# Optimization experiments

Measured on AMD Instinct MI355X. Metric: run time of the kernel, lower is better.

The kernel has to match this reference:

```python
import jax, jax.numpy as jnp
import numpy as np

# dims: batch, num queries, context len, model dim, heads, head dim,
# num_q_group, v_repeat, lora rank
B, NQ, NC, D = 4, 416, 257, 768
H, DH = 6, 128
G, R, LORA = 104, 4, 64  # NQ == R * G, all_q_mid == G * LORA
EPS = 1e-5


def ln(x, g, b):
    m = jnp.mean(x, axis=-1, keepdims=True)
    v = jnp.mean(jnp.square(x - m), axis=-1, keepdims=True)
    return (x - m) * jax.lax.rsqrt(v + EPS) * g + b


def setup_inputs() -> dict:
    key = jax.random.key(0)
    ks = jax.random.split(key, 7)
    s = 0.02
    return {
        "x": jax.random.normal(ks[0], (B, NQ, D), dtype=jnp.float32),
        "context": jax.random.normal(ks[1], (B, NC, D), dtype=jnp.float32),
        "Wq": jax.random.normal(ks[2], (D, D), dtype=jnp.float32) * s,
        "gq": jnp.ones((D,), jnp.float32), "bq": jnp.zeros((D,), jnp.float32),
        "Wk": jax.random.normal(ks[3], (D, D), dtype=jnp.float32) * s,
        "gk": jnp.ones((D,), jnp.float32), "bk": jnp.zeros((D,), jnp.float32),
        "Wv": jax.random.normal(ks[4], (D, G * LORA), dtype=jnp.float32) * s,
        "gv1": jnp.ones((G * LORA,), jnp.float32), "bv1": jnp.zeros((G * LORA,), jnp.float32),
        "Wconv": jax.random.normal(ks[5], (G, LORA, D), dtype=jnp.float32) * s,  # grouped 1x1 conv: per-group (LORA -> D)
        "gv2": jnp.ones((D,), jnp.float32), "bv2": jnp.zeros((D,), jnp.float32),
        "Wo": jax.random.normal(ks[6], (D, D), dtype=jnp.float32) * s,
        "go": jnp.ones((D,), jnp.float32), "bo": jnp.zeros((D,), jnp.float32),
    }


def reference(x, context, Wq, gq, bq, Wk, gk, bk, Wv, gv1, bv1, Wconv, gv2, bv2, Wo, go, bo):
    # to_q / to_k: Linear (no bias) + affine LayerNorm
    q = ln(x @ Wq, gq, bq)          # (B, NQ, D)
    k = ln(context @ Wk, gk, bk)    # (B, NC, D)
    # split heads -> (B*H, n, DH)
    q = q.reshape(B, NQ, H, DH).transpose(0, 2, 1, 3).reshape(B * H, NQ, DH)
    k = k.reshape(B, NC, H, DH).transpose(0, 2, 1, 3).reshape(B * H, NC, DH)

    # q-aware to_v: Linear -> LN -> grouped 1x1 Conv1d -> LN, plus skip of context
    mid = ln(context @ Wv, gv1, bv1)                 # (B, NC, G*LORA)
    mid = mid.reshape(B, NC, G, LORA)
    v = jnp.einsum('bngl,gld->bgnd', mid, Wconv)     # grouped conv, (B, G, NC, D)
    v = ln(v, gv2, bv2)
    v = v + context[:, None]                          # v_has_skip: context.unsqueeze(1)
    # heads: (B, G, NC, H, DH) -> (B*H, G, NC, DH)
    v = v.reshape(B, G, NC, H, DH).transpose(0, 3, 1, 2, 4).reshape(B * H, G, NC, DH)

    scale = DH ** (-0.25)
    sim = jnp.einsum('bid,bjd->bij', q * scale, k * scale)   # (B*H, NQ, NC)
    attn = jax.nn.softmax(sim, axis=-1)                       # dropout in eval mode: identity

    # torch repeat(1, R, 1, 1) tiles v along q-dim: query i uses group i % G.
    # reshape attn to (B*H, R, G, NC) so that i = r*G + g maps to group g.
    attn_g = attn.reshape(B * H, R, G, NC)
    out = jnp.einsum('brgj,bgjd->brgd', attn_g, v).reshape(B * H, NQ, DH)

    # merge heads -> (B, NQ, D)
    out = out.reshape(B, H, NQ, DH).transpose(0, 2, 1, 3).reshape(B, NQ, D)
    # to_out: Linear (no bias) + Dropout(eval: identity) + affine LayerNorm
    return ln(out @ Wo, go, bo)
```

## Files before the change

kernel.cpp:

```cpp
#include <hip/hip_runtime.h>


typedef unsigned short u16;
typedef unsigned int   u32;
typedef __attribute__((ext_vector_type(4))) float f32x4;
typedef __attribute__((ext_vector_type(4))) u32   u32x4;
typedef __attribute__((ext_vector_type(8))) short bf16x8;

__device__ __forceinline__ float bf2f(u16 v) { return __uint_as_float(((u32)v) << 16); }
__device__ __forceinline__ u16 f2bf(float f) {
  u32 u = __float_as_uint(f);
  u32 r = u + 0x7fffu + ((u >> 16) & 1u);
  return (u16)(r >> 16);
}
__device__ __forceinline__ float gld(const void* p, long idx, int f32) {
  return f32 ? ((const float*)p)[idx] : bf2f(((const u16*)p)[idx]);
}

typedef const __attribute__((address_space(1))) u32 gas_u32;
typedef __attribute__((address_space(3))) u32 las_u32;

__device__ __forceinline__ void stage16(const u16* g, u16* lbase, int lane) {
#if __has_builtin(__builtin_amdgcn_global_load_lds)
  (void)lane;
  __builtin_amdgcn_global_load_lds((gas_u32*)g, (las_u32*)lbase, 16, 0, 0);
#else
  *(u32x4*)(lbase + lane * 8) = *(const u32x4*)g;
#endif
}

__global__ __launch_bounds__(256) void probe_k(const u32* __restrict__ xw, int* __restrict__ flag) {
  int tid = threadIdx.x, c = 0;
  for (int i = tid; i < 4096; i += 256) {
    u16 lo = (u16)(xw[i] & 0xffffu);
    float a = fabsf(bf2f(lo));
    if (lo == 0 || (a >= 1e-3f && a <= 32.f)) ++c;
  }
#pragma unroll
  for (int o = 32; o; o >>= 1) c += __shfl_xor(c, o, 64);
  __shared__ int r[4];
  if ((tid & 63) == 0) r[tid >> 6] = c;
  __syncthreads();
  if (tid == 0) flag[0] = (r[0] + r[1] + r[2] + r[3] >= 2048) ? 0 : 1;
}

__global__ __launch_bounds__(256) void fill_k(u16* p, float v, int n) {
  int i = blockIdx.x * 256 + threadIdx.x;
  if (i < n) p[i] = f2bf(v);
}

__global__ __launch_bounds__(256) void convb4_k(
    const void* __restrict__ s0, u16* __restrict__ d0, int n0_,
    const void* __restrict__ s1, u16* __restrict__ d1, int n1_,
    const void* __restrict__ s2, u16* __restrict__ d2, int n2_,
    u16* __restrict__ midi, int n3_,
    const int* __restrict__ dtf)
{
  const int f = dtf[0];
  long i = ((long)blockIdx.x * 256 + threadIdx.x) * 8;
  const long t0 = n0_, t1 = t0 + n1_, t2 = t1 + n2_, t3 = t2 + n3_;
  if (i >= t3) return;
  if (i >= t2) {
    long e = i - t2;
    long z = e / 448, off = e - z * 448;
    u32x4 zz = {0u, 0u, 0u, 0u};
    *(u32x4*)(midi + z * 16896 + 16448 + off) = zz;
    return;
  }
  const void* in; u16* out;
  if (i < t0)      { in = s0; out = d0; }
  else if (i < t1) { in = s1; out = d1; i -= t0; }
  else             { in = s2; out = d2; i -= t1; }
  if (f) {
    const float* ip = (const float*)in + i;
    f32x4 a = *(const f32x4*)ip, b = *(const f32x4*)(ip + 4);
    u32x4 q = { (u32)f2bf(a.x) | ((u32)f2bf(a.y) << 16),
                (u32)f2bf(a.z) | ((u32)f2bf(a.w) << 16),
                (u32)f2bf(b.x) | ((u32)f2bf(b.y) << 16),
                (u32)f2bf(b.z) | ((u32)f2bf(b.w) << 16) };
    *(u32x4*)(out + i) = q;
  } else {
    *(u32x4*)(out + i) = *(const u32x4*)((const u16*)in + i);
  }
}

__global__ __launch_bounds__(256) void transM_k(
    const void* __restrict__ Wq, const void* __restrict__ Wk, const void* __restrict__ Wo,
    const void* __restrict__ Wv, const void* __restrict__ ctx,
    u16* __restrict__ wqt, u16* __restrict__ wkt, u16* __restrict__ wot,
    u16* __restrict__ wvt, u16* __restrict__ ctxT,
    const int* __restrict__ dtf)
{
  const int f = dtf[0];
  int t = blockIdx.x;
  const void* in; u16* out;
  int inK, inN, ldo, outK, nx;
  long inBase = 0, outBase = 0;
  if (t < 1728) {
    int w = t / 576; t -= w * 576;
    in  = w == 0 ? Wq : w == 1 ? Wk : Wo;
    out = w == 0 ? wqt : w == 1 ? wkt : wot;
    inK = 768; inN = 768; ldo = 768; outK = 768; nx = 24;
  } else if (t < 6720) {
    t -= 1728;
    in = Wv; out = wvt;
    inK = 768; inN = 6656; ldo = 768; outK = 768; nx = 208;
  } else {
    t -= 6720;
    int b = t / 216; t -= b * 216;
    in = ctx; out = ctxT;
    inK = 257; inN = 768; ldo = 264; outK = 264; nx = 24;
    inBase = (long)b * 257 * 768; outBase = (long)b * 768 * 264;
  }
  int n0 = (t % nx) * 32, k0 = (t / nx) * 32;
  __shared__ float s[32][33];
  int tx = threadIdx.x & 31, ty = threadIdx.x >> 5;
#pragma unroll
  for (int i = 0; i < 32; i += 8) {
    int k = k0 + ty + i, n = n0 + tx;
    float v = 0.f;
    if (k < inK && n < inN) v = gld(in, inBase + (long)k * inN + n, f);
    s[ty + i][tx] = v;
  }
  __syncthreads();
#pragma unroll
  for (int i = 0; i < 32; i += 8) {
    int n = n0 + ty + i, k = k0 + tx;
    if (n < inN && k < outK) out[outBase + (long)n * ldo + k] = f2bf(s[tx][ty + i]);
  }
}

__device__ __forceinline__ void gemm128_body(
    const u16* __restrict__ A, const u16* __restrict__ B, u16* __restrict__ C,
    int M, int N, int K, int lda, int ldb, int ldc, int m0, int n0)
{
  __shared__ __attribute__((aligned(16))) u16 As[128 * 32];
  __shared__ __attribute__((aligned(16))) u16 Bs[128 * 32];
  const int tid = threadIdx.x, lane = tid & 63, wave = tid >> 6;
  const int wm = (wave >> 1) * 64, wn = (wave & 1) * 64;
  const int fm = lane & 15, fq = lane >> 4;

  const int srow = lane >> 2, selem = (lane & 3) * 8;
  int ra1 = m0 + wave * 16 + srow;      if (ra1 > M - 1) ra1 = M - 1;
  int ra2 = m0 + 64 + wave * 16 + srow; if (ra2 > M - 1) ra2 = M - 1;
  const int rb1 = n0 + wave * 16 + srow;
  const int rb2 = n0 + 64 + wave * 16 + srow;
  const u16* pa1 = A + (long)ra1 * lda + selem;
  const u16* pa2 = A + (long)ra2 * lda + selem;
  const u16* pb1 = B + (long)rb1 * ldb + selem;
  const u16* pb2 = B + (long)rb2 * ldb + selem;
  u16* la1 = As + wave * 512;
  u16* la2 = As + 2048 + wave * 512;
  u16* lb1 = Bs + wave * 512;
  u16* lb2 = Bs + 2048 + wave * 512;

  f32x4 acc[4][4];
  const f32x4 zero4 = {0.f, 0.f, 0.f, 0.f};
#pragma unroll
  for (int a_ = 0; a_ < 4; ++a_)
#pragma unroll
    for (int b_ = 0; b_ < 4; ++b_) acc[a_][b_] = zero4;

  for (int k0 = 0; k0 < K; k0 += 32) {
    stage16(pa1, la1, lane);
    stage16(pa2, la2, lane);
    stage16(pb1, lb1, lane);
    stage16(pb2, lb2, lane);
    pa1 += 32; pa2 += 32; pb1 += 32; pb2 += 32;
    __syncthreads();
    bf16x8 fa[4], fb[4];
#pragma unroll
    for (int mt = 0; mt < 4; ++mt)
      fa[mt] = *(const bf16x8*)&As[(wm + mt * 16 + fm) * 32 + fq * 8];
#pragma unroll
    for (int nt = 0; nt < 4; ++nt)
      fb[nt] = *(const bf16x8*)&Bs[(wn + nt * 16 + fm) * 32 + fq * 8];
#pragma unroll
    for (int mt = 0; mt < 4; ++mt)
#pragma unroll
      for (int nt = 0; nt < 4; ++nt)
        acc[mt][nt] = __builtin_amdgcn_mfma_f32_16x16x32_bf16(fa[mt], fb[nt], acc[mt][nt], 0, 0, 0);
    __syncthreads();
  }
#pragma unroll
  for (int mt = 0; mt < 4; ++mt)
#pragma unroll
    for (int nt = 0; nt < 4; ++nt)
#pragma unroll
      for (int rr = 0; rr < 4; ++rr) {
        int gm = m0 + wm + mt * 16 + fq * 4 + rr;
        int gn = n0 + wn + nt * 16 + fm;
        if (gm < M) C[(long)gm * ldc + gn] = f2bf(acc[mt][nt][rr]);
      }
}

__global__ __launch_bounds__(256) void gemm128(
    const u16* __restrict__ A, const u16* __restrict__ B, u16* __restrict__ C,
    int M, int N, int K, int lda, int ldb, int ldc)
{
  gemm128_body(A, B, C, M, N, K, lda, ldb, ldc, blockIdx.x * 128, blockIdx.y * 128);
}

__global__ __launch_bounds__(256) void mgemm3_k(
    const u16* __restrict__ Aq, const u16* __restrict__ Bq, u16* __restrict__ Cq,
    const u16* __restrict__ Ak, const u16* __restrict__ Bk, u16* __restrict__ Ck,
    const u16* __restrict__ Am, const u16* __restrict__ Bm, u16* __restrict__ Cm)
{
  int bid = blockIdx.x;
  const u16 *A, *B; u16* C; int M, N, lid, mx;
  if (bid < 78)       { A = Aq; B = Bq; C = Cq; M = 1664; N = 768;  lid = bid;       mx = 13; }
  else if (bid < 132) { A = Ak; B = Bk; C = Ck; M = 1028; N = 768;  lid = bid - 78;  mx = 9;  }
  else                { A = Am; B = Bm; C = Cm; M = 1028; N = 6656; lid = bid - 132; mx = 9;  }
  int m0 = (lid % mx) * 128, n0 = (lid / mx) * 128;
  gemm128_body(A, B, C, M, N, 768, 768, 768, N, m0, n0);
}

#define LDS_S 40

__global__ __launch_bounds__(256) void gemm_bf16(
    const void* __restrict__ A, const void* __restrict__ B,
    float* __restrict__ Cf, u16* __restrict__ Cb, int obf,
    int M, int N, int K, int lda, int ldb, int ldc,
    long sAo, long sAi, int adiv, long sBo, long sBi, int bdiv,
    long sC, int zoff, int btrans, float alpha,
    const int* __restrict__ dtf, int aSel, int bSel)
{
  const int f = dtf[0];
  const int af32 = aSel & f, bf32 = bSel & f;
  const int zl = blockIdx.z, zg = zl + zoff;
  const long aoff = (long)(zg / adiv) * sAo + (long)(zg % adiv) * sAi;
  const long boff = (long)(zg / bdiv) * sBo + (long)(zg % bdiv) * sBi;
  const u16*   A16 = (const u16*)A + aoff;
  const float* A32 = (const float*)A + aoff;
  const u16*   B16 = (const u16*)B + boff;
  const float* B32 = (const float*)B + boff;

  __shared__ __attribute__((aligned(16))) u16 As[64 * LDS_S];
  __shared__ __attribute__((aligned(16))) u16 Bs[64 * LDS_S];

  const int tid = threadIdx.x;
  const int lane = tid & 63, wave = tid >> 6;
  const int m0 = blockIdx.x * 64, n0 = blockIdx.y * 64;
  const int wm = (wave >> 1) * 32, wn = (wave & 1) * 32;
  const int fm = lane & 15, fq = lane >> 4;

  const int ar = tid >> 2, ak = (tid & 3) * 8;
  const int bk = tid >> 3, bn = (tid & 7) * 8;

  f32x4 acc[2][2];
  const f32x4 zero4 = {0.f, 0.f, 0.f, 0.f};
#pragma unroll
  for (int a_ = 0; a_ < 2; ++a_)
#pragma unroll
    for (int b_ = 0; b_ < 2; ++b_) acc[a_][b_] = zero4;

  for (int k0 = 0; k0 < K; k0 += 32) {
    {
      int gm = m0 + ar, gk = k0 + ak;
      long idx = (long)gm * lda + gk;
      if (gm < M && gk + 8 <= K) {
        if (af32) {
          f32x4 u = *(const f32x4*)(A32 + idx), v = *(const f32x4*)(A32 + idx + 4);
          u32x4 q = { (u32)f2bf(u.x) | ((u32)f2bf(u.y) << 16),
                      (u32)f2bf(u.z) | ((u32)f2bf(u.w) << 16),
                      (u32)f2bf(v.x) | ((u32)f2bf(v.y) << 16),
                      (u32)f2bf(v.z) | ((u32)f2bf(v.w) << 16) };
          *(u32x4*)&As[ar * LDS_S + ak] = q;
        } else {
          *(u32x4*)&As[ar * LDS_S + ak] = *(const u32x4*)(A16 + idx);
        }
      } else {
#pragma unroll
        for (int e = 0; e < 8; ++e) {
          u16 v = 0;
          if (gm < M && gk + e < K) v = f2bf(gld(A, aoff + idx + e, af32));
          As[ar * LDS_S + ak + e] = v;
        }
      }
    }
    if (btrans) {
      int gn = n0 + ar, gk = k0 + ak;
      long idx = (long)gn * ldb + gk;
      if (gn < N && gk + 8 <= K) {
        if (bf32) {
          f32x4 u = *(const f32x4*)(B32 + idx), v = *(const f32x4*)(B32 + idx + 4);
          u32x4 q = { (u32)f2bf(u.x) | ((u32)f2bf(u.y) << 16),
                      (u32)f2bf(u.z) | ((u32)f2bf(u.w) << 16),
                      (u32)f2bf(v.x) | ((u32)f2bf(v.y) << 16),
                      (u32)f2bf(v.z) | ((u32)f2bf(v.w) << 16) };
          *(u32x4*)&Bs[ar * LDS_S + ak] = q;
        } else {
          *(u32x4*)&Bs[ar * LDS_S + ak] = *(const u32x4*)(B16 + idx);
        }
      } else {
#pragma unroll
        for (int e = 0; e < 8; ++e) {
          u16 v = 0;
          if (gn < N && gk + e < K) v = f2bf(gld(B, boff + idx + e, bf32));
          Bs[ar * LDS_S + ak + e] = v;
        }
      }
    } else {
      int gk = k0 + bk;
      long idx = (long)gk * ldb + n0 + bn;
      u16 tmp[8];
      if (gk < K) {
        if (bf32) {
          f32x4 u = *(const f32x4*)(B32 + idx), v = *(const f32x4*)(B32 + idx + 4);
          tmp[0] = f2bf(u.x); tmp[1] = f2bf(u.y); tmp[2] = f2bf(u.z); tmp[3] = f2bf(u.w);
          tmp[4] = f2bf(v.x); tmp[5] = f2bf(v.y); tmp[6] = f2bf(v.z); tmp[7] = f2bf(v.w);
        } else {
          u32x4 v = *(const u32x4*)(B16 + idx);
          tmp[0] = (u16)(v.x & 0xffff); tmp[1] = (u16)(v.x >> 16);
          tmp[2] = (u16)(v.y & 0xffff); tmp[3] = (u16)(v.y >> 16);
          tmp[4] = (u16)(v.z & 0xffff); tmp[5] = (u16)(v.z >> 16);
          tmp[6] = (u16)(v.w & 0xffff); tmp[7] = (u16)(v.w >> 16);
        }
      } else {
#pragma unroll
        for (int e = 0; e < 8; ++e) tmp[e] = 0;
      }
      int rot = tid & 7;
#pragma unroll
      for (int e = 0; e < 8; ++e) {
        int ee = (e + rot) & 7;
        Bs[(bn + ee) * LDS_S + bk] = tmp[ee];
      }
    }
    __syncthreads();
    {
      bf16x8 fa[2], fb[2];
      fa[0] = *(const bf16x8*)&As[(wm +      fm) * LDS_S + fq * 8];
      fa[1] = *(const bf16x8*)&As[(wm + 16 + fm) * LDS_S + fq * 8];
      fb[0] = *(const bf16x8*)&Bs[(wn +      fm) * LDS_S + fq * 8];
      fb[1] = *(const bf16x8*)&Bs[(wn + 16 + fm) * LDS_S + fq * 8];
#pragma unroll
      for (int mt = 0; mt < 2; ++mt)
#pragma unroll
        for (int nt = 0; nt < 2; ++nt)
          acc[mt][nt] = __builtin_amdgcn_mfma_f32_16x16x32_bf16(fa[mt], fb[nt], acc[mt][nt], 0, 0, 0);
    }
    __syncthreads();
  }
#pragma unroll
  for (int mt = 0; mt < 2; ++mt)
#pragma unroll
    for (int nt = 0; nt < 2; ++nt)
#pragma unroll
      for (int rr = 0; rr < 4; ++rr) {
        int gm = m0 + wm + mt * 16 + fq * 4 + rr;
        int gn = n0 + wn + nt * 16 + fm;
        if (gm < M && gn < N) {
          float v = alpha * acc[mt][nt][rr];
          if (obf) Cb[(long)zl * sC + (long)gm * ldc + gn] = f2bf(v);
          else     Cf[(long)zl * sC + (long)gm * ldc + gn] = v;
        }
      }
}

__device__ __forceinline__ void ln_row(
    const u16* __restrict__ ip, const void* __restrict__ g, const void* __restrict__ b,
    u16* __restrict__ ob, float* __restrict__ of, int N, int f)
{
  int tid = threadIdx.x, lane = tid & 63, wave = tid >> 6;
  const int nv = N >> 3;
  float s1 = 0.f, s2 = 0.f;
  for (int c8 = tid; c8 < nv; c8 += 256) {
    u32x4 v = *(const u32x4*)(ip + c8 * 8);
    float e0 = bf2f((u16)(v.x & 0xffff)), e1 = bf2f((u16)(v.x >> 16));
    float e2 = bf2f((u16)(v.y & 0xffff)), e3 = bf2f((u16)(v.y >> 16));
    float e4 = bf2f((u16)(v.z & 0xffff)), e5 = bf2f((u16)(v.z >> 16));
    float e6 = bf2f((u16)(v.w & 0xffff)), e7 = bf2f((u16)(v.w >> 16));
    s1 += ((e0 + e1) + (e2 + e3)) + ((e4 + e5) + (e6 + e7));
    s2 += ((e0*e0 + e1*e1) + (e2*e2 + e3*e3)) + ((e4*e4 + e5*e5) + (e6*e6 + e7*e7));
  }
#pragma unroll
  for (int o = 32; o; o >>= 1) { s1 += __shfl_xor(s1, o, 64); s2 += __shfl_xor(s2, o, 64); }
  __shared__ float red[8];
  if (lane == 0) { red[wave] = s1; red[4 + wave] = s2; }
  __syncthreads();
  s1 = red[0] + red[1] + red[2] + red[3];
  s2 = red[4] + red[5] + red[6] + red[7];
  float mean = s1 / N;
  float var = s2 / N - mean * mean;
  float rstd = rsqrtf(fmaxf(var, 0.f) + 1e-5f);
  for (int c8 = tid; c8 < nv; c8 += 256) {
    int c = c8 * 8;
    u32x4 v = *(const u32x4*)(ip + c);
    float e[8];
    e[0] = bf2f((u16)(v.x & 0xffff)); e[1] = bf2f((u16)(v.x >> 16));
    e[2] = bf2f((u16)(v.y & 0xffff)); e[3] = bf2f((u16)(v.y >> 16));
    e[4] = bf2f((u16)(v.z & 0xffff)); e[5] = bf2f((u16)(v.z >> 16));
    e[6] = bf2f((u16)(v.w & 0xffff)); e[7] = bf2f((u16)(v.w >> 16));
    float gg[8], bb[8];
    if (f) {
      const float* gp = (const float*)g + c; const float* bp = (const float*)b + c;
      f32x4 g0 = *(const f32x4*)gp, g1 = *(const f32x4*)(gp + 4);
      f32x4 b0 = *(const f32x4*)bp, b1 = *(const f32x4*)(bp + 4);
      gg[0]=g0.x; gg[1]=g0.y; gg[2]=g0.z; gg[3]=g0.w; gg[4]=g1.x; gg[5]=g1.y; gg[6]=g1.z; gg[7]=g1.w;
      bb[0]=b0.x; bb[1]=b0.y; bb[2]=b0.z; bb[3]=b0.w; bb[4]=b1.x; bb[5]=b1.y; bb[6]=b1.z; bb[7]=b1.w;
    } else {
      u32x4 gv = *(const u32x4*)((const u16*)g + c);
      u32x4 bv = *(const u32x4*)((const u16*)b + c);
      gg[0]=bf2f((u16)(gv.x&0xffff)); gg[1]=bf2f((u16)(gv.x>>16));
      gg[2]=bf2f((u16)(gv.y&0xffff)); gg[3]=bf2f((u16)(gv.y>>16));
      gg[4]=bf2f((u16)(gv.z&0xffff)); gg[5]=bf2f((u16)(gv.z>>16));
      gg[6]=bf2f((u16)(gv.w&0xffff)); gg[7]=bf2f((u16)(gv.w>>16));
      bb[0]=bf2f((u16)(bv.x&0xffff)); bb[1]=bf2f((u16)(bv.x>>16));
      bb[2]=bf2f((u16)(bv.y&0xffff)); bb[3]=bf2f((u16)(bv.y>>16));
      bb[4]=bf2f((u16)(bv.z&0xffff)); bb[5]=bf2f((u16)(bv.z>>16));
      bb[6]=bf2f((u16)(bv.w&0xffff)); bb[7]=bf2f((u16)(bv.w>>16));
    }
    float o_[8];
#pragma unroll
    for (int e2i = 0; e2i < 8; ++e2i) o_[e2i] = (e[e2i] - mean) * rstd * gg[e2i] + bb[e2i];
    if (of) {
      f32x4 o0 = {o_[0], o_[1], o_[2], o_[3]}, o1 = {o_[4], o_[5], o_[6], o_[7]};
      *(f32x4*)(of + c) = o0; *(f32x4*)(of + c + 4) = o1;
    } else {
      u32x4 q = { (u32)f2bf(o_[0]) | ((u32)f2bf(o_[1]) << 16),
                  (u32)f2bf(o_[2]) | ((u32)f2bf(o_[3]) << 16),
                  (u32)f2bf(o_[4]) | ((u32)f2bf(o_[5]) << 16),
                  (u32)f2bf(o_[6]) | ((u32)f2bf(o_[7]) << 16) };
      *(u32x4*)(ob + c) = q;
    }
  }
}

__global__ __launch_bounds__(256) void ln_rows(
    const u16* __restrict__ in, const void* __restrict__ g, const void* __restrict__ b,
    void* __restrict__ out, int N, const int* __restrict__ dtf, int isfinal)
{
  const int f = dtf[0];
  long row = blockIdx.x;
  const u16* ip = in + row * N;
  float* of = (isfinal && f) ? (float*)out + row * N : nullptr;
  u16*   ob = of ? nullptr : (u16*)out + row * N;
  ln_row(ip, g, b, ob, of, N, f);
}

__global__ __launch_bounds__(256) void mln3_k(
    u16* __restrict__ qb, const void* __restrict__ gq, const void* __restrict__ bq,
    u16* __restrict__ kb, const void* __restrict__ gk, const void* __restrict__ bk,
    u16* __restrict__ mb, const void* __restrict__ gv, const void* __restrict__ bv,
    const int* __restrict__ dtf)
{
  const int f = dtf[0];
  int row = blockIdx.x;
  u16* ip; const void *g, *b; int N;
  if (row < 1664)      { ip = qb + (long)row * 768; g = gq; b = bq; N = 768; }
  else if (row < 2692) { ip = kb + (long)(row - 1664) * 768; g = gk; b = bk; N = 768; }
  else                 { ip = mb + (long)(row - 2692) * 6656; g = gv; b = bv; N = 6656; }
  ln_row(ip, g, b, ip, nullptr, N, f);
}

__global__ __launch_bounds__(256) void wbar_k(const u16* __restrict__ Wb,
                                              float* __restrict__ wbar)
{
  int r = blockIdx.x * 4 + (threadIdx.x >> 6);
  int lane = threadIdx.x & 63;
  const u16* p = Wb + (long)r * 768;
  float s = 0.f;
  for (int c = lane; c < 768; c += 64) s += bf2f(p[c]);
#pragma unroll
  for (int o = 32; o; o >>= 1) s += __shfl_xor(s, o, 64);
  if (lane == 0) wbar[r] = s * (1.f / 768.f);
}

__global__ __launch_bounds__(256) void stats2_k(
    const u16* __restrict__ midbf, const u16* __restrict__ Y, const float* __restrict__ wbar,
    u16* __restrict__ midi, float* __restrict__ pim)
{
  int g = blockIdx.y;
  int r = blockIdx.x * 4 + (threadIdx.x >> 6);
  int lane = threadIdx.x & 63;
  int b = r / 257, j = r - b * 257;
  float m = bf2f(midbf[(long)r * 6656 + g * 64 + lane]);
  float y = bf2f(Y[((long)g * 1028 + r) * 64 + lane]);
  float wb = wbar[g * 64 + lane];
  float mup = m * wb, q2p = m * y;
#pragma unroll
  for (int o = 32; o; o >>= 1) { mup += __shfl_xor(mup, o, 64); q2p += __shfl_xor(q2p, o, 64); }
  float var = q2p - mup * mup;
  float inv = rsqrtf(fmaxf(var, 0.f) + 1e-5f);
  long zidx = (long)b * 104 + g;
  midi[(zidx * 264 + j) * 64 + lane] = f2bf(inv * m);
  if (lane == 0) pim[zidx * 257 + j] = inv * mup;
}

__global__ __launch_bounds__(256) void softmax_k(
    const float* __restrict__ simf, const float* __restrict__ pim,
    u16* __restrict__ Abf, u16* __restrict__ A2bf, float* __restrict__ s_sh)
{
  int bh = blockIdx.x;
  int b = bh / 6, h = bh - b * 6;
  int tid = threadIdx.x, lane = tid & 63, wave = tid >> 6;
  int i = blockIdx.y * 4 + wave;
  int g = i % 104, rq = i / 104;
  const float* sp_ = simf + ((long)bh * 416 + i) * 257;
  float s[5];
#pragma unroll
  for (int jc = 0; jc < 5; ++jc) {
    int j = jc * 64 + lane;
    s[jc] = (j < 257) ? sp_[j] : -1e30f;
  }
  float mx = -1e30f;
#pragma unroll
  for (int jc = 0; jc < 5; ++jc) mx = fmaxf(mx, s[jc]);
#pragma unroll
  for (int o = 32; o; o >>= 1) mx = fmaxf(mx, __shfl_xor(mx, o, 64));
  float p[5], sum = 0.f, sp = 0.f;
  long pimb = ((long)b * 104 + g) * 257;
#pragma unroll
  for (int jc = 0; jc < 5; ++jc) {
    int j = jc * 64 + lane;
    float pv = 0.f;
    if (j < 257) { pv = __expf(s[jc] - mx); sp = fmaf(pv, pim[pimb + j], sp); }
    p[jc] = pv; sum += pv;
  }
#pragma unroll
  for (int o = 32; o; o >>= 1) { sum += __shfl_xor(sum, o, 64); sp += __shfl_xor(sp, o, 64); }
  float rs = 1.f / sum;
  long arow  = ((long)bh * 416 + i) * 264;
  long a2row = (((long)b * 104 + g) * 24 + h * 4 + rq) * 264;
#pragma unroll
  for (int jc = 0; jc < 5; ++jc) {
    int j = jc * 64 + lane;
    if (j < 257) { u16 pb = f2bf(p[jc] * rs); Abf[arow + j] = pb; A2bf[a2row + j] = pb; }
    else if (j < 264) { Abf[arow + j] = 0; A2bf[a2row + j] = 0; }
  }
  if (lane == 0) s_sh[(long)bh * 416 + i] = sp * rs;
}

__global__ __launch_bounds__(256) void oc_k(
    const u16* __restrict__ T, const u16* __restrict__ Wb,
    const float* __restrict__ s_sh, const float* __restrict__ c_buf,
    const void* __restrict__ gv2, const void* __restrict__ bv2,
    u16* __restrict__ opbf, const int* __restrict__ dtf)
{
  const int f = dtf[0];
  int z = blockIdx.x;
  int b = z / 104, g = z - b * 104;
  int tid = threadIdx.x;
  __shared__ float Ts[24][64];
  const u16* tp = T + (long)z * 1536;
  for (int idx = tid; idx < 1536; idx += 256) Ts[idx >> 6][idx & 63] = bf2f(tp[idx]);
  __syncthreads();
  const int dh = tid & 127;
  const int hbase = (tid >> 7) * 3;
  const u16* wg = Wb + (long)g * 49152;
#pragma unroll
  for (int hh = 0; hh < 3; ++hh) {
    int h = hbase + hh;
    int d = h * 128 + dh;
    const u16* wp = wg + d;
    float a0 = 0.f, a1 = 0.f, a2 = 0.f, a3 = 0.f;
#pragma unroll 16
    for (int k = 0; k < 64; ++k) {
      float w = bf2f(wp[(long)k * 768]);
      a0 = fmaf(Ts[h * 4 + 0][k], w, a0);
      a1 = fmaf(Ts[h * 4 + 1][k], w, a1);
      a2 = fmaf(Ts[h * 4 + 2][k], w, a2);
      a3 = fmaf(Ts[h * 4 + 3][k], w, a3);
    }
    float acc[4] = {a0, a1, a2, a3};
    float gvd = gld(gv2, d, f), bvd = gld(bv2, d, f);
#pragma unroll
    for (int rq = 0; rq < 4; ++rq) {
      int i = rq * 104 + g;
      float ssh = s_sh[((long)b * 6 + h) * 416 + i];
      float val = gvd * (acc[rq] - ssh) + bvd
                + c_buf[(((long)b * 6 + h) * 416 + i) * 128 + dh];
      opbf[((long)b * 416 + i) * 768 + d] = f2bf(val);
    }
  }
}

static void launch_gemm(const void* A, const void* B, float* Cf, u16* Cb, int obf,
                        int M, int N, int K, int lda, int ldb, int ldc,
                        long sAo, long sAi, int adiv, long sBo, long sBi, int bdiv,
                        long sC, int zoff, int Z, int btrans, float alpha,
                        const int* dtf, int aSel, int bSel, hipStream_t st)
{
  dim3 grid((M + 63) / 64, (N + 63) / 64, Z);
  gemm_bf16<<<grid, dim3(256), 0, st>>>(A, B, Cf, Cb, obf, M, N, K, lda, ldb, ldc,
                                        sAo, sAi, adiv, sBo, sBi, bdiv,
                                        sC, zoff, btrans, alpha, dtf, aSel, bSel);
}

extern "C" void kernel_launch(void* const* d_in, const int* in_sizes, int n_in,
                              void* d_out, int out_size, void* d_ws, size_t ws_size,
                              hipStream_t stream)
{
  (void)in_sizes; (void)n_in;
  const void* x   = d_in[0];
  const void* ctx = d_in[1];
  const void* Wq  = d_in[2];
  const void* gq  = d_in[3];
  const void* bq  = d_in[4];
  const void* Wk  = d_in[5];
  const void* gk  = d_in[6];
  const void* bk  = d_in[7];
  const void* Wv  = d_in[8];
  const void* gv1 = d_in[9];
  const void* bv1 = d_in[10];
  const void* Wcv = d_in[11];
  const void* gv2 = d_in[12];
  const void* bv2 = d_in[13];
  const void* Wo  = d_in[14];
  const void* go  = d_in[15];
  const void* bo  = d_in[16];

  const size_t SZ_FLAG = 256;
  const size_t SZ_QBF  = 2555904;
  const size_t SZ_KBF  = 1579008;
  const size_t SZ_MID  = 13684736;
  const size_t SZ_MM   = 1703936;
  const size_t SZ_WB   = 26624;
  const size_t SZ_MIDI = 14057472;
  const size_t SZ_PIM  = 427648;
  const size_t SZ_ABF  = 5271552;
  const size_t SZ_A2   = 5271552;
  const size_t SZ_SSH  = 39936;
  const size_t SZ_CB   = 1579008;
  const size_t SZ_WCVB = 10223616;
  const size_t SZ_YF   = 13684736;
  const size_t SZ_WT   = 1179648;
  const size_t SZ_WVT  = 10223616;
  const size_t SZ_CTXT = 1622016;
  const size_t REQUIRED = SZ_FLAG + SZ_QBF + SZ_KBF + SZ_MID + SZ_MM + SZ_WB +
                          SZ_MIDI + SZ_PIM + SZ_ABF + SZ_A2 + SZ_SSH + SZ_CB +
                          SZ_WCVB + SZ_YF + 3 * SZ_WT + SZ_WVT + SZ_CTXT;

  if (ws_size < REQUIRED) {
    fill_k<<<(out_size + 255) / 256, 256, 0, stream>>>((u16*)d_out, (float)(ws_size >> 20), out_size);
    return;
  }

  char* p = (char*)d_ws;
  int*   dtf   = (int*)  p;                 p += SZ_FLAG;
  u16*   qbf   = (u16*)  p;                 p += SZ_QBF;
  u16*   kbf   = (u16*)  p;                 p += SZ_KBF;
  char*  midrg = p;                         p += SZ_MID;
  char*  mmrg  = p;                         p += SZ_MM;
  float* wbar  = (float*)p;                 p += SZ_WB;
  u16*   midi  = (u16*)  p;                 p += SZ_MIDI;
  float* pim   = (float*)p;                 p += SZ_PIM;
  char*  abfrg = p;                         p += SZ_ABF;
  u16*   A2bf  = (u16*)  p;                 p += SZ_A2;
  float* s_sh  = (float*)p;                 p += SZ_SSH;
  u16*   cb    = (u16*)  p;                 p += SZ_CB;
  u16*   wcvb  = (u16*)  p;                 p += SZ_WCVB;
  u16*   yfull = (u16*)  p;                 p += SZ_YF;
  u16*   wqt2  = (u16*)  p;                 p += SZ_WT;
  u16*   wkt2  = (u16*)  p;                 p += SZ_WT;
  u16*   wot2  = (u16*)  p;                 p += SZ_WT;
  u16*   wvt   = (u16*)  p;                 p += SZ_WVT;
  u16*   ctxT  = (u16*)  p;                 p += SZ_CTXT;

  u16*   midbf = (u16*)midrg;
  float* simf  = (float*)midrg;
  float* c_buf = (float*)midrg;
  u16*   Tb16  = (u16*)(midrg + 5111808);
  u16*   Gb    = (u16*)mmrg;
  u16*   xb    = (u16*)abfrg;
  u16*   Abf   = (u16*)abfrg;
  u16*   opbf  = (u16*)abfrg;

  probe_k<<<1, 256, 0, stream>>>((const u32*)x, dtf);

  {
    const int n0_ = 1277952, n1_ = 789504, n2_ = 5111808, n3_ = 186368;
    long tot = (long)n0_ + n1_ + n2_ + n3_;
    int blocks = (int)((tot / 8 + 255) / 256);
    convb4_k<<<blocks, 256, 0, stream>>>(x, xb, n0_, ctx, cb, n1_, Wcv, wcvb, n2_,
                                         midi, n3_, dtf);
  }
  transM_k<<<7584, 256, 0, stream>>>(Wq, Wk, Wo, Wv, ctx,
                                     wqt2, wkt2, wot2, wvt, ctxT, dtf);

  mgemm3_k<<<600, 256, 0, stream>>>(xb, wqt2, qbf, cb, wkt2, kbf, cb, wvt, midbf);
  mln3_k<<<3720, 256, 0, stream>>>(qbf, gq, bq, kbf, gk, bk, midbf, gv1, bv1, dtf);

  launch_gemm(wcvb, wcvb, nullptr, Gb, 1, 64, 64, 768, 768, 768, 64,
              49152, 0, 1, 49152, 0, 1, 4096, 0, 104, 1, 1.f / 768.f, dtf, 0, 0, stream);
  wbar_k<<<1664, 256, 0, stream>>>(wcvb, wbar);
  launch_gemm(midbf, Gb, nullptr, yfull, 1,
              1028, 64, 64, 6656, 64, 64,
              0, 64, 104, 4096, 0, 1, 65792, 0, 104, 1, 1.f, dtf, 0, 0, stream);
  stats2_k<<<dim3(257, 104), 256, 0, stream>>>(midbf, yfull, wbar, midi, pim);

  launch_gemm(qbf, kbf, simf, nullptr, 0, 416, 257, 128, 768, 768, 257,
              319488, 128, 6, 197376, 128, 6, 106912, 0, 24, 1,
              0.08838834764831845f, dtf, 0, 0, stream);
  softmax_k<<<dim3(24, 104), 256, 0, stream>>>(simf, pim, Abf, A2bf, s_sh);

  launch_gemm(Abf, ctxT, c_buf, nullptr, 0, 416, 128, 264, 264, 264, 128,
              109824, 0, 1, 202752, 33792, 6, 53248, 0, 24, 1, 1.f, dtf, 0, 0, stream);
  launch_gemm(A2bf, midi, nullptr, Tb16, 1, 24, 64, 264, 264, 64, 64,
              6336, 0, 1, 16896, 0, 1, 1536, 0, 416, 0, 1.f, dtf, 0, 0, stream);

  oc_k<<<416, 256, 0, stream>>>(Tb16, wcvb, s_sh, c_buf, gv2, bv2, opbf, dtf);

  {
    dim3 grid(13, 6, 1);
    gemm128<<<grid, dim3(256), 0, stream>>>(opbf, wot2, qbf, 1664, 768, 768, 768, 768, 768);
  }
  ln_rows<<<1664, 256, 0, stream>>>(qbf, go, bo, d_out, 768, dtf, 1);
}
```

Measured before the change: 309.1 us.

## Merge independent launches into combined multi-role kernels to cut launch count

Folds the conversion, transpose and wbar kernels into one prep kernel. It merges the Gram GEMM into the projection GEMM launch, the Y GEMM with the QK^T sim GEMM, and the two attention-output GEMMs into one launch each. The sim buffer gets its own workspace region so it no longer aliases midbf while both are live. The aim is fewer kernel launches and less inter-kernel idle time, at the cost of heterogeneous blocks and the loss of the fp32 input path in the generic GEMM.

After: 273.2 us. 11.6% less time.

```diff
diff --git a/kernel.cpp b/kernel.cpp
--- a/kernel.cpp
+++ b/kernel.cpp
@@ -49,84 +49,92 @@
   if (i < n) p[i] = f2bf(v);
 }
 
-__global__ __launch_bounds__(256) void convb4_k(
-    const void* __restrict__ s0, u16* __restrict__ d0, int n0_,
-    const void* __restrict__ s1, u16* __restrict__ d1, int n1_,
-    const void* __restrict__ s2, u16* __restrict__ d2, int n2_,
-    u16* __restrict__ midi, int n3_,
-    const int* __restrict__ dtf)
-{
-  const int f = dtf[0];
-  long i = ((long)blockIdx.x * 256 + threadIdx.x) * 8;
-  const long t0 = n0_, t1 = t0 + n1_, t2 = t1 + n2_, t3 = t2 + n3_;
-  if (i >= t3) return;
-  if (i >= t2) {
-    long e = i - t2;
-    long z = e / 448, off = e - z * 448;
-    u32x4 zz = {0u, 0u, 0u, 0u};
-    *(u32x4*)(midi + z * 16896 + 16448 + off) = zz;
-    return;
-  }
-  const void* in; u16* out;
-  if (i < t0)      { in = s0; out = d0; }
-  else if (i < t1) { in = s1; out = d1; i -= t0; }
-  else             { in = s2; out = d2; i -= t1; }
-  if (f) {
-    const float* ip = (const float*)in + i;
-    f32x4 a = *(const f32x4*)ip, b = *(const f32x4*)(ip + 4);
-    u32x4 q = { (u32)f2bf(a.x) | ((u32)f2bf(a.y) << 16),
-                (u32)f2bf(a.z) | ((u32)f2bf(a.w) << 16),
-                (u32)f2bf(b.x) | ((u32)f2bf(b.y) << 16),
-                (u32)f2bf(b.z) | ((u32)f2bf(b.w) << 16) };
-    *(u32x4*)(out + i) = q;
-  } else {
-    *(u32x4*)(out + i) = *(const u32x4*)((const u16*)in + i);
-  }
-}
-
-__global__ __launch_bounds__(256) void transM_k(
-    const void* __restrict__ Wq, const void* __restrict__ Wk, const void* __restrict__ Wo,
-    const void* __restrict__ Wv, const void* __restrict__ ctx,
+__global__ __launch_bounds__(256) void prep_k(
+    const void* __restrict__ x,   u16* __restrict__ xb,
+    const void* __restrict__ ctx, u16* __restrict__ cbuf,
+    const void* __restrict__ Wcv, u16* __restrict__ wcvb,
+    u16* __restrict__ midi,
+    const void* __restrict__ Wq, const void* __restrict__ Wk,
+    const void* __restrict__ Wo, const void* __restrict__ Wv,
     u16* __restrict__ wqt, u16* __restrict__ wkt, u16* __restrict__ wot,
     u16* __restrict__ wvt, u16* __restrict__ ctxT,
-    const int* __restrict__ dtf)
+    float* __restrict__ wbar, const int* __restrict__ dtf)
 {
   const int f = dtf[0];
-  int t = blockIdx.x;
-  const void* in; u16* out;
-  int inK, inN, ldo, outK, nx;
-  long inBase = 0, outBase = 0;
-  if (t < 1728) {
-    int w = t / 576; t -= w * 576;
-    in  = w == 0 ? Wq : w == 1 ? Wk : Wo;
-    out = w == 0 ? wqt : w == 1 ? wkt : wot;
-    inK = 768; inN = 768; ldo = 768; outK = 768; nx = 24;
-  } else if (t < 6720) {
-    t -= 1728;
-    in = Wv; out = wvt;
-    inK = 768; inN = 6656; ldo = 768; outK = 768; nx = 208;
+  int bid = blockIdx.x;
+  __shared__ float s[32][33];
+  if (bid < 3597) {
+    const long n0_ = 1277952, n1_ = 789504, n2_ = 5111808, n3_ = 186368;
+    long i = ((long)bid * 256 + threadIdx.x) * 8;
+    const long t0 = n0_, t1 = t0 + n1_, t2 = t1 + n2_, t3 = t2 + n3_;
+    if (i >= t3) return;
+    if (i >= t2) {
+      long e = i - t2;
+      long z = e / 448, off = e - z * 448;
+      u32x4 zz = {0u, 0u, 0u, 0u};
+      *(u32x4*)(midi + z * 16896 + 16448 + off) = zz;
+      return;
+    }
+    const void* in; u16* out;
+    if (i < t0)      { in = x;    out = xb; }
+    else if (i < t1) { in = ctx;  out = cbuf; i -= t0; }
+    else             { in = Wcv;  out = wcvb; i -= t1; }
+    if (f) {
+      const float* ip = (const float*)in + i;
+      f32x4 a = *(const f32x4*)ip, b = *(const f32x4*)(ip + 4);
+      u32x4 q = { (u32)f2bf(a.x) | ((u32)f2bf(a.y) << 16),
+                  (u32)f2bf(a.z) | ((u32)f2bf(a.w) << 16),
+                  (u32)f2bf(b.x) | ((u32)f2bf(b.y) << 16),
+                  (u32)f2bf(b.z) | ((u32)f2bf(b.w) << 16) };
+      *(u32x4*)(out + i) = q;
+    } else {
+      *(u32x4*)(out + i) = *(const u32x4*)((const u16*)in + i);
+    }
+  } else if (bid < 11181) {
+    int t = bid - 3597;
+    const void* in; u16* out;
+    int inK, inN, ldo, outK, nx;
+    long inBase = 0, outBase = 0;
+    if (t < 1728) {
+      int w = t / 576; t -= w * 576;
+      in  = w == 0 ? Wq : w == 1 ? Wk : Wo;
+      out = w == 0 ? wqt : w == 1 ? wkt : wot;
+      inK = 768; inN = 768; ldo = 768; outK = 768; nx = 24;
+    } else if (t < 6720) {
+      t -= 1728;
+      in = Wv; out = wvt;
+      inK = 768; inN = 6656; ldo = 768; outK = 768; nx = 208;
+    } else {
+      t -= 6720;
+      int b = t / 216; t -= b * 216;
+      in = ctx; out = ctxT;
+      inK = 257; inN = 768; ldo = 264; outK = 264; nx = 24;
+      inBase = (long)b * 257 * 768; outBase = (long)b * 768 * 264;
+    }
+    int n0 = (t % nx) * 32, k0 = (t / nx) * 32;
+    int tx = threadIdx.x & 31, ty = threadIdx.x >> 5;
+#pragma unroll
+    for (int i = 0; i < 32; i += 8) {
+      int k = k0 + ty + i, n = n0 + tx;
+      float v = 0.f;
+      if (k < inK && n < inN) v = gld(in, inBase + (long)k * inN + n, f);
+      s[ty + i][tx] = v;
+    }
+    __syncthreads();
+#pragma unroll
+    for (int i = 0; i < 32; i += 8) {
+      int n = n0 + ty + i, k = k0 + tx;
+      if (n < inN && k < outK) out[outBase + (long)n * ldo + k] = f2bf(s[tx][ty + i]);
+    }
   } else {
-    t -= 6720;
-    int b = t / 216; t -= b * 216;
-    in = ctx; out = ctxT;
-    inK = 257; inN = 768; ldo = 264; outK = 264; nx = 24;
-    inBase = (long)b * 257 * 768; outBase = (long)b * 768 * 264;
-  }
-  int n0 = (t % nx) * 32, k0 = (t / nx) * 32;
-  __shared__ float s[32][33];
-  int tx = threadIdx.x & 31, ty = threadIdx.x >> 5;
-#pragma unroll
-  for (int i = 0; i < 32; i += 8) {
-    int k = k0 + ty + i, n = n0 + tx;
-    float v = 0.f;
-    if (k < inK && n < inN) v = gld(in, inBase + (long)k * inN + n, f);
-    s[ty + i][tx] = v;
-  }
-  __syncthreads();
-#pragma unroll
-  for (int i = 0; i < 32; i += 8) {
-    int n = n0 + ty + i, k = k0 + tx;
-    if (n < inN && k < outK) out[outBase + (long)n * ldo + k] = f2bf(s[tx][ty + i]);
+    int r = (bid - 11181) * 4 + (threadIdx.x >> 6);
+    int lane = threadIdx.x & 63;
+    long base = (long)r * 768;
+    float sm = 0.f;
+    for (int c = lane; c < 768; c += 64) sm += gld(Wcv, base + c, f);
+#pragma unroll
+    for (int o = 32; o; o >>= 1) sm += __shfl_xor(sm, o, 64);
+    if (lane == 0) wbar[r] = sm * (1.f / 768.f);
   }
 }
 
@@ -201,49 +209,19 @@
   gemm128_body(A, B, C, M, N, K, lda, ldb, ldc, blockIdx.x * 128, blockIdx.y * 128);
 }
 
-__global__ __launch_bounds__(256) void mgemm3_k(
-    const u16* __restrict__ Aq, const u16* __restrict__ Bq, u16* __restrict__ Cq,
-    const u16* __restrict__ Ak, const u16* __restrict__ Bk, u16* __restrict__ Ck,
-    const u16* __restrict__ Am, const u16* __restrict__ Bm, u16* __restrict__ Cm)
-{
-  int bid = blockIdx.x;
-  const u16 *A, *B; u16* C; int M, N, lid, mx;
-  if (bid < 78)       { A = Aq; B = Bq; C = Cq; M = 1664; N = 768;  lid = bid;       mx = 13; }
-  else if (bid < 132) { A = Ak; B = Bk; C = Ck; M = 1028; N = 768;  lid = bid - 78;  mx = 9;  }
-  else                { A = Am; B = Bm; C = Cm; M = 1028; N = 6656; lid = bid - 132; mx = 9;  }
-  int m0 = (lid % mx) * 128, n0 = (lid / mx) * 128;
-  gemm128_body(A, B, C, M, N, 768, 768, 768, N, m0, n0);
-}
-
 #define LDS_S 40
 
-__global__ __launch_bounds__(256) void gemm_bf16(
-    const void* __restrict__ A, const void* __restrict__ B,
-    float* __restrict__ Cf, u16* __restrict__ Cb, int obf,
+__device__ __forceinline__ void gemm64_body(
+    u16* As, u16* Bs,
+    const u16* __restrict__ A16, const u16* __restrict__ B16,
+    float* Cf, u16* Cb,
     int M, int N, int K, int lda, int ldb, int ldc,
-    long sAo, long sAi, int adiv, long sBo, long sBi, int bdiv,
-    long sC, int zoff, int btrans, float alpha,
-    const int* __restrict__ dtf, int aSel, int bSel)
-{
-  const int f = dtf[0];
-  const int af32 = aSel & f, bf32 = bSel & f;
-  const int zl = blockIdx.z, zg = zl + zoff;
-  const long aoff = (long)(zg / adiv) * sAo + (long)(zg % adiv) * sAi;
-  const long boff = (long)(zg / bdiv) * sBo + (long)(zg % bdiv) * sBi;
-  const u16*   A16 = (const u16*)A + aoff;
-  const float* A32 = (const float*)A + aoff;
-  const u16*   B16 = (const u16*)B + boff;
-  const float* B32 = (const float*)B + boff;
-
-  __shared__ __attribute__((aligned(16))) u16 As[64 * LDS_S];
-  __shared__ __attribute__((aligned(16))) u16 Bs[64 * LDS_S];
-
+    int btrans, float alpha, int m0, int n0)
+{
   const int tid = threadIdx.x;
   const int lane = tid & 63, wave = tid >> 6;
-  const int m0 = blockIdx.x * 64, n0 = blockIdx.y * 64;
   const int wm = (wave >> 1) * 32, wn = (wave & 1) * 32;
   const int fm = lane & 15, fq = lane >> 4;
-
   const int ar = tid >> 2, ak = (tid & 3) * 8;
   const int bk = tid >> 3, bn = (tid & 7) * 8;
 
@@ -259,63 +237,33 @@
       int gm = m0 + ar, gk = k0 + ak;
       long idx = (long)gm * lda + gk;
       if (gm < M && gk + 8 <= K) {
-        if (af32) {
-          f32x4 u = *(const f32x4*)(A32 + idx), v = *(const f32x4*)(A32 + idx + 4);
-          u32x4 q = { (u32)f2bf(u.x) | ((u32)f2bf(u.y) << 16),
-                      (u32)f2bf(u.z) | ((u32)f2bf(u.w) << 16),
-                      (u32)f2bf(v.x) | ((u32)f2bf(v.y) << 16),
-                      (u32)f2bf(v.z) | ((u32)f2bf(v.w) << 16) };
-          *(u32x4*)&As[ar * LDS_S + ak] = q;
-        } else {
-          *(u32x4*)&As[ar * LDS_S + ak] = *(const u32x4*)(A16 + idx);
-        }
+        *(u32x4*)&As[ar * LDS_S + ak] = *(const u32x4*)(A16 + idx);
       } else {
 #pragma unroll
-        for (int e = 0; e < 8; ++e) {
-          u16 v = 0;
-          if (gm < M && gk + e < K) v = f2bf(gld(A, aoff + idx + e, af32));
-          As[ar * LDS_S + ak + e] = v;
-        }
+        for (int e = 0; e < 8; ++e)
+          As[ar * LDS_S + ak + e] = (gm < M && gk + e < K) ? A16[idx + e] : (u16)0;
       }
     }
     if (btrans) {
       int gn = n0 + ar, gk = k0 + ak;
       long idx = (long)gn * ldb + gk;
       if (gn < N && gk + 8 <= K) {
-        if (bf32) {
-          f32x4 u = *(const f32x4*)(B32 + idx), v = *(const f32x4*)(B32 + idx + 4);
-          u32x4 q = { (u32)f2bf(u.x) | ((u32)f2bf(u.y) << 16),
-                      (u32)f2bf(u.z) | ((u32)f2bf(u.w) << 16),
-                      (u32)f2bf(v.x) | ((u32)f2bf(v.y) << 16),
-                      (u32)f2bf(v.z) | ((u32)f2bf(v.w) << 16) };
-          *(u32x4*)&Bs[ar * LDS_S + ak] = q;
-        } else {
-          *(u32x4*)&Bs[ar * LDS_S + ak] = *(const u32x4*)(B16 + idx);
-        }
+        *(u32x4*)&Bs[ar * LDS_S + ak] = *(const u32x4*)(B16 + idx);
       } else {
 #pragma unroll
-        for (int e = 0; e < 8; ++e) {
-          u16 v = 0;
-          if (gn < N && gk + e < K) v = f2bf(gld(B, boff + idx + e, bf32));
-          Bs[ar * LDS_S + ak + e] = v;
-        }
+        for (int e = 0; e < 8; ++e)
+          Bs[ar * LDS_S + ak + e] = (gn < N && gk + e < K) ? B16[idx + e] : (u16)0;
       }
     } else {
       int gk = k0 + bk;
       long idx = (long)gk * ldb + n0 + bn;
       u16 tmp[8];
       if (gk < K) {
-        if (bf32) {
-          f32x4 u = *(const f32x4*)(B32 + idx), v = *(const f32x4*)(B32 + idx + 4);
-          tmp[0] = f2bf(u.x); tmp[1] = f2bf(u.y); tmp[2] = f2bf(u.z); tmp[3] = f2bf(u.w);
-          tmp[4] = f2bf(v.x); tmp[5] = f2bf(v.y); tmp[6] = f2bf(v.z); tmp[7] = f2bf(v.w);
-        } else {
-          u32x4 v = *(const u32x4*)(B16 + idx);
-          tmp[0] = (u16)(v.x & 0xffff); tmp[1] = (u16)(v.x >> 16);
-          tmp[2] = (u16)(v.y & 0xffff); tmp[3] = (u16)(v.y >> 16);
-          tmp[4] = (u16)(v.z & 0xffff); tmp[5] = (u16)(v.z >> 16);
-          tmp[6] = (u16)(v.w & 0xffff); tmp[7] = (u16)(v.w >> 16);
-        }
+        u32x4 v = *(const u32x4*)(B16 + idx);
+        tmp[0] = (u16)(v.x & 0xffff); tmp[1] = (u16)(v.x >> 16);
+        tmp[2] = (u16)(v.y & 0xffff); tmp[3] = (u16)(v.y >> 16);
+        tmp[4] = (u16)(v.z & 0xffff); tmp[5] = (u16)(v.z >> 16);
+        tmp[6] = (u16)(v.w & 0xffff); tmp[7] = (u16)(v.w >> 16);
       } else {
 #pragma unroll
         for (int e = 0; e < 8; ++e) tmp[e] = 0;
@@ -352,10 +300,86 @@
         int gn = n0 + wn + nt * 16 + fm;
         if (gm < M && gn < N) {
           float v = alpha * acc[mt][nt][rr];
-          if (obf) Cb[(long)zl * sC + (long)gm * ldc + gn] = f2bf(v);
-          else     Cf[(long)zl * sC + (long)gm * ldc + gn] = v;
+          if (Cb) Cb[(long)gm * ldc + gn] = f2bf(v);
+          else    Cf[(long)gm * ldc + gn] = v;
         }
       }
+}
+
+__global__ __launch_bounds__(256) void mg4_k(
+    const u16* __restrict__ xb, const u16* __restrict__ wqt, u16* __restrict__ qbf,
+    const u16* __restrict__ cbuf, const u16* __restrict__ wkt, u16* __restrict__ kbf,
+    const u16* __restrict__ wvt, u16* __restrict__ midbf,
+    const u16* __restrict__ wcvb, u16* __restrict__ Gb)
+{
+  int bid = blockIdx.x;
+  if (bid < 600) {
+    const u16 *A, *B; u16* C; int M, N, lid, mx;
+    if (bid < 78)       { A = xb;   B = wqt; C = qbf;   M = 1664; N = 768;  lid = bid;       mx = 13; }
+    else if (bid < 132) { A = cbuf; B = wkt; C = kbf;   M = 1028; N = 768;  lid = bid - 78;  mx = 9;  }
+    else                { A = cbuf; B = wvt; C = midbf; M = 1028; N = 6656; lid = bid - 132; mx = 9;  }
+    int m0 = (lid % mx) * 128, n0 = (lid / mx) * 128;
+    gemm128_body(A, B, C, M, N, 768, 768, 768, N, m0, n0);
+  } else {
+    __shared__ __attribute__((aligned(16))) u16 As[64 * LDS_S];
+    __shared__ __attribute__((aligned(16))) u16 Bs[64 * LDS_S];
+    int z = bid - 600;
+    gemm64_body(As, Bs, wcvb + (long)z * 49152, wcvb + (long)z * 49152,
+                nullptr, Gb + (long)z * 4096,
+                64, 64, 768, 768, 768, 64, 1, 1.f / 768.f, 0, 0);
+  }
+}
+
+__global__ __launch_bounds__(256) void ysim_k(
+    const u16* __restrict__ midbf, const u16* __restrict__ Gb, u16* __restrict__ yfull,
+    const u16* __restrict__ qbf, const u16* __restrict__ kbf, float* __restrict__ simf)
+{
+  __shared__ __attribute__((aligned(16))) u16 As[64 * LDS_S];
+  __shared__ __attribute__((aligned(16))) u16 Bs[64 * LDS_S];
+  int bid = blockIdx.x;
+  const u16 *A, *B; float* Cf = nullptr; u16* Cb = nullptr;
+  int M, N, K, lda, ldb, ldc, btrans, m0, n0; float alpha;
+  if (bid < 1768) {
+    int z = bid / 17, bx = bid % 17;
+    A = midbf + (long)z * 64;  B = Gb + (long)z * 4096;  Cb = yfull + (long)z * 65792;
+    M = 1028; N = 64; K = 64; lda = 6656; ldb = 64; ldc = 64;
+    btrans = 1; alpha = 1.f; m0 = bx * 64; n0 = 0;
+  } else {
+    int lid = bid - 1768; int z = lid / 35, r = lid % 35, bx = r % 7, by = r / 7;
+    A = qbf + (long)(z / 6) * 319488 + (long)(z % 6) * 128;
+    B = kbf + (long)(z / 6) * 197376 + (long)(z % 6) * 128;
+    Cf = simf + (long)z * 106912;
+    M = 416; N = 257; K = 128; lda = 768; ldb = 768; ldc = 257;
+    btrans = 1; alpha = 0.08838834764831845f; m0 = bx * 64; n0 = by * 64;
+  }
+  gemm64_body(As, Bs, A, B, Cf, Cb, M, N, K, lda, ldb, ldc, btrans, alpha, m0, n0);
+}
+
+__global__ __launch_bounds__(256) void ct_k(
+    const u16* __restrict__ Abf, const u16* __restrict__ ctxT, float* __restrict__ c_buf,
+    const u16* __restrict__ A2bf, const u16* __restrict__ midi, u16* __restrict__ Tb16)
+{
+  __shared__ __attribute__((aligned(16))) u16 As[64 * LDS_S];
+  __shared__ __attribute__((aligned(16))) u16 Bs[64 * LDS_S];
+  int bid = blockIdx.x;
+  const u16 *A, *B; float* Cf = nullptr; u16* Cb = nullptr;
+  int M, N, K, lda, ldb, ldc, btrans, m0, n0; float alpha;
+  if (bid < 336) {
+    int z = bid / 14, r = bid % 14, bx = r % 7, by = r / 7;
+    A = Abf + (long)z * 109824;
+    B = ctxT + (long)(z / 6) * 202752 + (long)(z % 6) * 33792;
+    Cf = c_buf + (long)z * 53248;
+    M = 416; N = 128; K = 264; lda = 264; ldb = 264; ldc = 128;
+    btrans = 1; alpha = 1.f; m0 = bx * 64; n0 = by * 64;
+  } else {
+    int z = bid - 336;
+    A = A2bf + (long)z * 6336;
+    B = midi + (long)z * 16896;
+    Cb = Tb16 + (long)z * 1536;
+    M = 24; N = 64; K = 264; lda = 264; ldb = 64; ldc = 64;
+    btrans = 0; alpha = 1.f; m0 = 0; n0 = 0;
+  }
+  gemm64_body(As, Bs, A, B, Cf, Cb, M, N, K, lda, ldb, ldc, btrans, alpha, m0, n0);
 }
 
 __device__ __forceinline__ void ln_row(
@@ -454,19 +478,6 @@
   ln_row(ip, g, b, ip, nullptr, N, f);
 }
 
-__global__ __launch_bounds__(256) void wbar_k(const u16* __restrict__ Wb,
-                                              float* __restrict__ wbar)
-{
-  int r = blockIdx.x * 4 + (threadIdx.x >> 6);
-  int lane = threadIdx.x & 63;
-  const u16* p = Wb + (long)r * 768;
-  float s = 0.f;
-  for (int c = lane; c < 768; c += 64) s += bf2f(p[c]);
-#pragma unroll
-  for (int o = 32; o; o >>= 1) s += __shfl_xor(s, o, 64);
-  if (lane == 0) wbar[r] = s * (1.f / 768.f);
-}
-
 __global__ __launch_bounds__(256) void stats2_k(
     const u16* __restrict__ midbf, const u16* __restrict__ Y, const float* __restrict__ wbar,
     u16* __restrict__ midi, float* __restrict__ pim)
@@ -574,18 +585,6 @@
       opbf[((long)b * 416 + i) * 768 + d] = f2bf(val);
     }
   }
-}
-
-static void launch_gemm(const void* A, const void* B, float* Cf, u16* Cb, int obf,
-                        int M, int N, int K, int lda, int ldb, int ldc,
-                        long sAo, long sAi, int adiv, long sBo, long sBi, int bdiv,
-                        long sC, int zoff, int Z, int btrans, float alpha,
-                        const int* dtf, int aSel, int bSel, hipStream_t st)
-{
-  dim3 grid((M + 63) / 64, (N + 63) / 64, Z);
-  gemm_bf16<<<grid, dim3(256), 0, st>>>(A, B, Cf, Cb, obf, M, N, K, lda, ldb, ldc,
-                                        sAo, sAi, adiv, sBo, sBi, bdiv,
-                                        sC, zoff, btrans, alpha, dtf, aSel, bSel);
 }
 
 extern "C" void kernel_launch(void* const* d_in, const int* in_sizes, int n_in,
@@ -628,9 +627,10 @@
   const size_t SZ_WT   = 1179648;
   const size_t SZ_WVT  = 10223616;
   const size_t SZ_CTXT = 1622016;
+  const size_t SZ_SIMF = 10263552;
   const size_t REQUIRED = SZ_FLAG + SZ_QBF + SZ_KBF + SZ_MID + SZ_MM + SZ_WB +
                           SZ_MIDI + SZ_PIM + SZ_ABF + SZ_A2 + SZ_SSH + SZ_CB +
-                          SZ_WCVB + SZ_YF + 3 * SZ_WT + SZ_WVT + SZ_CTXT;
+                          SZ_WCVB + SZ_YF + 3 * SZ_WT + SZ_WVT + SZ_CTXT + SZ_SIMF;
 
   if (ws_size < REQUIRED) {
     fill_k<<<(out_size + 255) / 256, 256, 0, stream>>>((u16*)d_out, (float)(ws_size >> 20), out_size);
@@ -657,9 +657,9 @@
   u16*   wot2  = (u16*)  p;                 p += SZ_WT;
   u16*   wvt   = (u16*)  p;                 p += SZ_WVT;
   u16*   ctxT  = (u16*)  p;                 p += SZ_CTXT;
+  float* simf  = (float*)p;                 p += SZ_SIMF;
 
   u16*   midbf = (u16*)midrg;
-  float* simf  = (float*)midrg;
   float* c_buf = (float*)midrg;
   u16*   Tb16  = (u16*)(midrg + 5111808);
   u16*   Gb    = (u16*)mmrg;
@@ -669,36 +669,20 @@
 
   probe_k<<<1, 256, 0, stream>>>((const u32*)x, dtf);
 
-  {
-    const int n0_ = 1277952, n1_ = 789504, n2_ = 5111808, n3_ = 186368;
-    long tot = (long)n0_ + n1_ + n2_ + n3_;
-    int blocks = (int)((tot / 8 + 255) / 256);
-    convb4_k<<<blocks, 256, 0, stream>>>(x, xb, n0_, ctx, cb, n1_, Wcv, wcvb, n2_,
-                                         midi, n3_, dtf);
-  }
-  transM_k<<<7584, 256, 0, stream>>>(Wq, Wk, Wo, Wv, ctx,
-                                     wqt2, wkt2, wot2, wvt, ctxT, dtf);
-
-  mgemm3_k<<<600, 256, 0, stream>>>(xb, wqt2, qbf, cb, wkt2, kbf, cb, wvt, midbf);
+  prep_k<<<12845, 256, 0, stream>>>(x, xb, ctx, cb, Wcv, wcvb, midi,
+                                    Wq, Wk, Wo, Wv, wqt2, wkt2, wot2, wvt, ctxT,
+                                    wbar, dtf);
+
+  mg4_k<<<704, 256, 0, stream>>>(xb, wqt2, qbf, cb, wkt2, kbf, wvt, midbf, wcvb, Gb);
+
   mln3_k<<<3720, 256, 0, stream>>>(qbf, gq, bq, kbf, gk, bk, midbf, gv1, bv1, dtf);
 
-  launch_gemm(wcvb, wcvb, nullptr, Gb, 1, 64, 64, 768, 768, 768, 64,
-              49152, 0, 1, 49152, 0, 1, 4096, 0, 104, 1, 1.f / 768.f, dtf, 0, 0, stream);
-  wbar_k<<<1664, 256, 0, stream>>>(wcvb, wbar);
-  launch_gemm(midbf, Gb, nullptr, yfull, 1,
-              1028, 64, 64, 6656, 64, 64,
-              0, 64, 104, 4096, 0, 1, 65792, 0, 104, 1, 1.f, dtf, 0, 0, stream);
+  ysim_k<<<2608, 256, 0, stream>>>(midbf, Gb, yfull, qbf, kbf, simf);
+
   stats2_k<<<dim3(257, 104), 256, 0, stream>>>(midbf, yfull, wbar, midi, pim);
-
-  launch_gemm(qbf, kbf, simf, nullptr, 0, 416, 257, 128, 768, 768, 257,
-              319488, 128, 6, 197376, 128, 6, 106912, 0, 24, 1,
-              0.08838834764831845f, dtf, 0, 0, stream);
   softmax_k<<<dim3(24, 104), 256, 0, stream>>>(simf, pim, Abf, A2bf, s_sh);
 
-  launch_gemm(Abf, ctxT, c_buf, nullptr, 0, 416, 128, 264, 264, 264, 128,
-              109824, 0, 1, 202752, 33792, 6, 53248, 0, 24, 1, 1.f, dtf, 0, 0, stream);
-  launch_gemm(A2bf, midi, nullptr, Tb16, 1, 24, 64, 264, 264, 64, 64,
-              6336, 0, 1, 16896, 0, 1, 1536, 0, 416, 0, 1.f, dtf, 0, 0, stream);
+  ct_k<<<752, 256, 0, stream>>>(Abf, ctxT, c_buf, A2bf, midi, Tb16);
 
   oc_k<<<416, 256, 0, stream>>>(Tb16, wcvb, s_sh, c_buf, gv2, bv2, opbf, dtf);
 
```
